# Kernel optimization log

Measured on AMD Instinct MI355X. Metric: run time of the kernel, lower is better.

## Reference

```python
import jax, jax.numpy as jnp
import numpy as np
import math

EMBED_DIM = 1024
N_HEADS = 16
QK_DIM = 64
V_DIM = 64
B, S = 4, 2048


def setup_inputs() -> dict:
    key = jax.random.key(0)
    ks = jax.random.split(key, 10)
    sc = lambda fan_in: 1.0 / math.sqrt(fan_in)
    X = jax.random.normal(ks[0], (B, S, EMBED_DIM), dtype=jnp.float32)
    mask = jax.random.randint(ks[1], (B, 1, S, S), 0, 2, dtype=jnp.int32)
    wQ = jax.random.uniform(ks[2], (EMBED_DIM, QK_DIM * N_HEADS), jnp.float32, -sc(EMBED_DIM), sc(EMBED_DIM))
    bQ = jnp.zeros((QK_DIM * N_HEADS,), jnp.float32)
    wK = jax.random.uniform(ks[3], (EMBED_DIM, QK_DIM * N_HEADS), jnp.float32, -sc(EMBED_DIM), sc(EMBED_DIM))
    bK = jnp.zeros((QK_DIM * N_HEADS,), jnp.float32)
    wV = jax.random.uniform(ks[4], (EMBED_DIM, V_DIM * N_HEADS), jnp.float32, -sc(EMBED_DIM), sc(EMBED_DIM))
    bV = jnp.zeros((V_DIM * N_HEADS,), jnp.float32)
    wO = jax.random.uniform(ks[5], (V_DIM * N_HEADS, EMBED_DIM), jnp.float32, -sc(V_DIM * N_HEADS), sc(V_DIM * N_HEADS))
    bO = jnp.zeros((EMBED_DIM,), jnp.float32)
    return {"X": X, "mask": mask, "wQ": wQ, "bQ": bQ, "wK": wK, "bK": bK,
            "wV": wV, "bV": bV, "wO": wO, "bO": bO}


def reference(X, mask, wQ, bQ, wK, bK, wV, bV, wO, bO):
    Bsz, Slen, _ = X.shape
    # projections -> [B, H, S, d]
    q = (X @ wQ + bQ).reshape(Bsz, Slen, N_HEADS, QK_DIM).transpose(0, 2, 1, 3)
    k = (X @ wK + bK).reshape(Bsz, Slen, N_HEADS, QK_DIM).transpose(0, 2, 1, 3)
    v = (X @ wV + bV).reshape(Bsz, Slen, N_HEADS, V_DIM).transpose(0, 2, 1, 3)
    # scores [B, H, S, S]
    scores = jnp.einsum("bhqd,bhkd->bhqk", q, k) / math.sqrt(QK_DIM)
    scores = jnp.where(mask == 0, jnp.float32(-1e9), scores)
    probs = jax.nn.softmax(scores, axis=-1)
    out = jnp.einsum("bhqk,bhkd->bhqd", probs, v)  # [B, H, S, v]
    out = out.transpose(0, 2, 1, 3).reshape(Bsz, Slen, N_HEADS * V_DIM)
    return out @ wO + bO
```

## Files before the change

### kernel.cpp

```cpp
#include <hip/hip_runtime.h>
#include <hip/hip_bf16.h>

#define EMB 1024
#define NH 16
#define DH 64
#define SEQ 2048

typedef __attribute__((ext_vector_type(8))) __bf16 bf16x8;
typedef __attribute__((ext_vector_type(4))) float f32x4;
typedef __attribute__((ext_vector_type(16))) float f32x16;

__device__ __forceinline__ void g2l16(const void* g, void* l) {
  __builtin_amdgcn_global_load_lds(
      (const __attribute__((address_space(1))) void*)g,
      (__attribute__((address_space(3))) void*)l, 16, 0, 0);
}

__global__ void detect_k(const unsigned short* __restrict__ xs,
                         int* __restrict__ flag) {
  __shared__ int cnt;
  if (threadIdx.x == 0) cnt = 0;
  __syncthreads();
  int hits = 0;
  for (int i = threadIdx.x; i < 16384; i += 256) {
    unsigned e = (xs[i] >> 7) & 0xFFu;
    if (e >= 0xC0u) hits++;
  }
  atomicAdd(&cnt, hits);
  __syncthreads();
  if (threadIdx.x == 0) *flag = (cnt > 16) ? 1 : 0;
}

__global__ void conv_k(const void* __restrict__ src,
                       __hip_bfloat16* __restrict__ dst,
                       const int* __restrict__ flag, int n4) {
  int i = blockIdx.x * 256 + threadIdx.x;
  if (i >= n4) return;
  if (*flag) {
    float4 v = ((const float4*)src)[i];
    ushort4 o;
    __hip_bfloat16 t;
    t = __float2bfloat16(v.x); o.x = *(unsigned short*)&t;
    t = __float2bfloat16(v.y); o.y = *(unsigned short*)&t;
    t = __float2bfloat16(v.z); o.z = *(unsigned short*)&t;
    t = __float2bfloat16(v.w); o.w = *(unsigned short*)&t;
    ((ushort4*)dst)[i] = o;
  } else {
    ((ushort4*)dst)[i] = ((const ushort4*)src)[i];
  }
}

__global__ void convB_k(const void* s0, const void* s1, const void* s2,
                        const void* s3, __hip_bfloat16* __restrict__ dst,
                        const int* __restrict__ flag) {
  const void* srcs[4] = {s0, s1, s2, s3};
  const void* src = srcs[blockIdx.x];
  int i = threadIdx.x;
  __hip_bfloat16* d = dst + blockIdx.x * 1024;
  if (*flag) {
    float4 v = ((const float4*)src)[i];
    ushort4 o;
    __hip_bfloat16 t;
    t = __float2bfloat16(v.x); o.x = *(unsigned short*)&t;
    t = __float2bfloat16(v.y); o.y = *(unsigned short*)&t;
    t = __float2bfloat16(v.z); o.z = *(unsigned short*)&t;
    t = __float2bfloat16(v.w); o.w = *(unsigned short*)&t;
    ((ushort4*)d)[i] = o;
  } else {
    ((ushort4*)d)[i] = ((const ushort4*)src)[i];
  }
}

__global__ void transW4_k(const void* s0, const void* s1, const void* s2,
                          const void* s3, __hip_bfloat16* d0,
                          __hip_bfloat16* d1, __hip_bfloat16* d2,
                          __hip_bfloat16* d3, const int* __restrict__ flag) {
  __shared__ __hip_bfloat16 tile[32][33];
  const void* srcs[4] = {s0, s1, s2, s3};
  __hip_bfloat16* dsts[4] = {d0, d1, d2, d3};
  const void* src = srcs[blockIdx.z];
  __hip_bfloat16* dst = dsts[blockIdx.z];
  int f = *flag;
  int tx = threadIdx.x, ty = threadIdx.y;
  int x = blockIdx.x * 32 + tx;
  int y0 = blockIdx.y * 32;
  for (int i = 0; i < 32; i += 8) {
    int idx = (y0 + ty + i) * EMB + x;
    tile[ty + i][tx] = f ? __float2bfloat16(((const float*)src)[idx])
                         : ((const __hip_bfloat16*)src)[idx];
  }
  __syncthreads();
  int x2 = y0 + tx;
  int y2 = blockIdx.x * 32;
  for (int i = 0; i < 32; i += 8)
    dst[(size_t)(y2 + ty + i) * EMB + x2] = tile[tx][ty + i];
}

__global__ void maskpack_k(const int* __restrict__ mask,
                           unsigned int* __restrict__ bits) {
  int g = blockIdx.x * 256 + threadIdx.x;
  int lane = threadIdx.x & 63;
  unsigned long long bal = __ballot(mask[g] != 0);
  if ((lane & 31) == 0)
    bits[g >> 5] = (unsigned int)(bal >> (lane & 32));
}

__launch_bounds__(256)
__global__ void gemm_qkv(const __hip_bfloat16* __restrict__ A,
                         const __hip_bfloat16* __restrict__ Bt,
                         const __hip_bfloat16* __restrict__ bias,
                         __hip_bfloat16* __restrict__ CQ,
                         __hip_bfloat16* __restrict__ CK,
                         __hip_bfloat16* __restrict__ CV) {
  __shared__ __align__(16) __bf16 sA[128 * 32];
  __shared__ __align__(16) __bf16 sB[128 * 32];
  const __bf16* Ab = (const __bf16*)A;
  const __bf16* Bb = (const __bf16*)Bt;

  int tid = threadIdx.x;
  int w = tid >> 6, lane = tid & 63;
  int quad = lane >> 4, lcol = lane & 15;
  int m0 = blockIdx.x * 128, n0 = blockIdx.y * 128;
  int wm = (w >> 1) * 64, wn = (w & 1) * 64;
  int region = n0 >> 10;

  f32x4 z = {0.f, 0.f, 0.f, 0.f};
  f32x4 acc[4][4];
#pragma unroll
  for (int i = 0; i < 4; i++)
#pragma unroll
    for (int j = 0; j < 4; j++) acc[i][j] = z;

  int c = w * 64 + lane;
  int r = c >> 2, cc = c & 3;

  for (int k0 = 0; k0 < 1024; k0 += 32) {
    __syncthreads();
    g2l16(Ab + (size_t)(m0 + r) * 1024 + k0 + cc * 8, (char*)sA + w * 1024);
    g2l16(Ab + (size_t)(m0 + r + 64) * 1024 + k0 + cc * 8, (char*)sA + 4096 + w * 1024);
    g2l16(Bb + (size_t)(n0 + r) * 1024 + k0 + cc * 8, (char*)sB + w * 1024);
    g2l16(Bb + (size_t)(n0 + r + 64) * 1024 + k0 + cc * 8, (char*)sB + 4096 + w * 1024);
    __syncthreads();

    bf16x8 af[4], bfr[4];
#pragma unroll
    for (int i = 0; i < 4; i++)
      af[i] = *(const bf16x8*)(sA + (wm + i * 16 + lcol) * 32 + quad * 8);
#pragma unroll
    for (int j = 0; j < 4; j++)
      bfr[j] = *(const bf16x8*)(sB + (wn + j * 16 + lcol) * 32 + quad * 8);
#pragma unroll
    for (int i = 0; i < 4; i++)
#pragma unroll
      for (int j = 0; j < 4; j++)
        acc[i][j] = __builtin_amdgcn_mfma_f32_16x16x32_bf16(af[i], bfr[j], acc[i][j], 0, 0, 0);
  }

  float scale = (region == 0) ? 0.18033688011111204f : 1.0f;
#pragma unroll
  for (int j = 0; j < 4; j++) {
    int col = n0 + wn + j * 16 + lcol;
    float bv = __bfloat162float(bias[col]);
    int lc = col & 1023;
    int h = lc >> 6, dd = lc & 63;
#pragma unroll
    for (int i = 0; i < 4; i++) {
      int rbase = m0 + wm + i * 16 + quad * 4;
      int b = rbase >> 11, s = rbase & 2047;
      if (region == 1) {
#pragma unroll
        for (int rr = 0; rr < 4; rr++) {
          float v = acc[i][j][rr] + bv;
          CK[(((size_t)(b * NH + h)) * SEQ + s + rr) * DH + dd] = __float2bfloat16(v);
        }
      } else {
        union { unsigned long long u; __hip_bfloat16 bb[4]; } pk;
#pragma unroll
        for (int rr = 0; rr < 4; rr++)
          pk.bb[rr] = __float2bfloat16((acc[i][j][rr] + bv) * scale);
        __hip_bfloat16* dst = (region == 0) ? CQ : CV;
        *(unsigned long long*)(dst + (((size_t)(b * NH + h)) * DH + dd) * SEQ + s) = pk.u;
      }
    }
  }
}

__launch_bounds__(256)
__global__ void gemm_o(const __hip_bfloat16* __restrict__ A,
                       const __hip_bfloat16* __restrict__ Bt,
                       const __hip_bfloat16* __restrict__ bias,
                       void* __restrict__ Cv, const int* __restrict__ flag) {
  __shared__ __align__(16) __bf16 sA[128 * 32];
  __shared__ __align__(16) __bf16 sB[128 * 32];
  const __bf16* Ab = (const __bf16*)A;
  const __bf16* Bb = (const __bf16*)Bt;
  int f32out = *flag;

  int tid = threadIdx.x;
  int w = tid >> 6, lane = tid & 63;
  int quad = lane >> 4, lcol = lane & 15;
  int m0 = blockIdx.x * 128, n0 = blockIdx.y * 128;
  int wm = (w >> 1) * 64, wn = (w & 1) * 64;

  f32x4 z = {0.f, 0.f, 0.f, 0.f};
  f32x4 acc[4][4];
#pragma unroll
  for (int i = 0; i < 4; i++)
#pragma unroll
    for (int j = 0; j < 4; j++) acc[i][j] = z;

  int c = w * 64 + lane;
  int r = c >> 2, cc = c & 3;

  for (int k0 = 0; k0 < 1024; k0 += 32) {
    __syncthreads();
    g2l16(Ab + (size_t)(m0 + r) * 1024 + k0 + cc * 8, (char*)sA + w * 1024);
    g2l16(Ab + (size_t)(m0 + r + 64) * 1024 + k0 + cc * 8, (char*)sA + 4096 + w * 1024);
    g2l16(Bb + (size_t)(n0 + r) * 1024 + k0 + cc * 8, (char*)sB + w * 1024);
    g2l16(Bb + (size_t)(n0 + r + 64) * 1024 + k0 + cc * 8, (char*)sB + 4096 + w * 1024);
    __syncthreads();

    bf16x8 af[4], bfr[4];
#pragma unroll
    for (int i = 0; i < 4; i++)
      af[i] = *(const bf16x8*)(sA + (wm + i * 16 + lcol) * 32 + quad * 8);
#pragma unroll
    for (int j = 0; j < 4; j++)
      bfr[j] = *(const bf16x8*)(sB + (wn + j * 16 + lcol) * 32 + quad * 8);
#pragma unroll
    for (int i = 0; i < 4; i++)
#pragma unroll
      for (int j = 0; j < 4; j++)
        acc[i][j] = __builtin_amdgcn_mfma_f32_16x16x32_bf16(af[i], bfr[j], acc[i][j], 0, 0, 0);
  }

#pragma unroll
  for (int j = 0; j < 4; j++) {
    int col = n0 + wn + j * 16 + lcol;
    float bv = __bfloat162float(bias[col]);
#pragma unroll
    for (int i = 0; i < 4; i++) {
      int rbase = m0 + wm + i * 16 + quad * 4;
#pragma unroll
      for (int rr = 0; rr < 4; rr++) {
        int m = rbase + rr;
        float v = acc[i][j][rr] + bv;
        if (f32out)
          ((float*)Cv)[(size_t)m * EMB + col] = v;
        else
          ((__hip_bfloat16*)Cv)[(size_t)m * EMB + col] = __float2bfloat16(v);
      }
    }
  }
}

__launch_bounds__(256, 4)
__global__ void attn_k(const __hip_bfloat16* __restrict__ Qt,
                       const __hip_bfloat16* __restrict__ Kp,
                       const __hip_bfloat16* __restrict__ Vp,
                       const unsigned int* __restrict__ mbits,
                       __hip_bfloat16* __restrict__ AO) {
  __shared__ __align__(16) __bf16 sK[2 * 64 * 64];
  __shared__ __align__(16) __bf16 sV[2 * 64 * 64];
  __shared__ unsigned long long sLut[16];

  int tid = threadIdx.x;
  int w = tid >> 6, lane = tid & 63, hi = lane >> 5, l31 = lane & 31;
  int swz7 = l31 & 7;
  int bid = blockIdx.x;
  int xcd = bid & 7, idx = bid >> 3;
  int bh = xcd * 8 + (idx >> 4);
  int qblk = idx & 15;
  int b = bh >> 4, h = bh & 15;

  if (tid < 16) {
    unsigned long long v = 0;
    if (tid & 1) v |= 0xFFFFull;
    if (tid & 2) v |= 0xFFFFull << 16;
    if (tid & 4) v |= 0xFFFFull << 32;
    if (tid & 8) v |= 0xFFFFull << 48;
    sLut[tid] = v;
  }

  const __bf16* Qb = (const __bf16*)Qt + (size_t)bh * DH * SEQ;
  const __bf16* Kb = (const __bf16*)Kp + (size_t)bh * SEQ * DH;
  const __bf16* Vb = (const __bf16*)Vp + (size_t)bh * DH * SEQ;
  int q_mine = qblk * 128 + w * 32 + l31;

  union { bf16x8 v; __bf16 e[8]; } qf[4];
#pragma unroll
  for (int s = 0; s < 4; s++)
#pragma unroll
    for (int j = 0; j < 8; j++)
      qf[s].e[j] = Qb[(size_t)(s * 16 + hi * 8 + j) * SEQ + q_mine];

  __bf16 onev = (__bf16)1.0f;
  bf16x8 ones = {onev, onev, onev, onev, onev, onev, onev, onev};

  f32x16 z16 = {0.f, 0.f, 0.f, 0.f, 0.f, 0.f, 0.f, 0.f,
                0.f, 0.f, 0.f, 0.f, 0.f, 0.f, 0.f, 0.f};
  f32x16 ot0 = z16, ot1 = z16;
  f32x16 lacc = z16;

  const unsigned long long* mrow =
      (const unsigned long long*)mbits + ((size_t)b * SEQ + q_mine) * (SEQ / 64);

  int kr = lane >> 3, pc = lane & 7;

  auto STAGE = [&](int buf, int kt) {
#pragma unroll
    for (int t2 = 0; t2 < 2; t2++) {
      int row = w * 16 + t2 * 8 + kr;
      g2l16(Kb + (size_t)(kt * 64 + row) * DH + (pc ^ kr) * 8,
            (char*)sK + buf * 8192 + (w * 16 + t2 * 8) * 128);
      g2l16(Vb + (size_t)row * SEQ + kt * 64 + (pc ^ kr) * 8,
            (char*)sV + buf * 8192 + (w * 16 + t2 * 8) * 128);
    }
  };

  STAGE(0, 0);
  unsigned long long mb = mrow[0];
  __syncthreads();

  for (int kt = 0; kt < SEQ / 64; ++kt) {
    int cur = kt & 1;
    const char* sKc = (const char*)sK + cur * 8192;
    const char* sVc = (const char*)sV + cur * 8192;
    if (kt < SEQ / 64 - 1) STAGE(cur ^ 1, kt + 1);
    unsigned long long mb_next = mrow[(kt + 1) & (SEQ / 64 - 1)];
    unsigned long long mbc = mb >> (4 * hi);

#pragma unroll
    for (int ct = 0; ct < 2; ct++) {
      f32x16 sc = z16;
      __builtin_amdgcn_s_setprio(1);
#pragma unroll
      for (int s = 0; s < 4; s++) {
        bf16x8 a = *(const bf16x8*)(sKc + ct * 4096 + l31 * 128 +
                                    (((2 * s + hi) ^ swz7) << 4));
        sc = __builtin_amdgcn_mfma_f32_32x32x16_bf16(a, qf[s].v, sc, 0, 0, 0);
      }
      __builtin_amdgcn_s_setprio(0);

      unsigned long long pr[4];
#pragma unroll
      for (int g = 0; g < 4; g++) {
        union { unsigned long long u; __bf16 bb[4]; } pk;
#pragma unroll
        for (int r = 0; r < 4; r++)
          pk.bb[r] = (__bf16)__builtin_amdgcn_exp2f(sc[4 * g + r]);
        unsigned nib = (unsigned)(mbc >> (32 * ct + 8 * g)) & 0xFu;
        pr[g] = pk.u & sLut[nib];
      }

      __builtin_amdgcn_s_setprio(1);
#pragma unroll
      for (int f2 = 0; f2 < 2; f2++) {
        int kb = 2 * ct + f2;
        union { bf16x8 v; unsigned long long d2[2]; } bp;
        bp.d2[0] = pr[2 * f2];
        bp.d2[1] = pr[2 * f2 + 1];
        int ch0 = ((2 * kb) ^ swz7) << 4;
        int ch1 = ((2 * kb + 1) ^ swz7) << 4;
        union { bf16x8 v; unsigned long long d2[2]; } av0, av1;
        const char* vr0 = sVc + l31 * 128 + 8 * hi;
        const char* vr1 = sVc + (32 + l31) * 128 + 8 * hi;
        av0.d2[0] = *(const unsigned long long*)(vr0 + ch0);
        av0.d2[1] = *(const unsigned long long*)(vr0 + ch1);
        av1.d2[0] = *(const unsigned long long*)(vr1 + ch0);
        av1.d2[1] = *(const unsigned long long*)(vr1 + ch1);
        ot0 = __builtin_amdgcn_mfma_f32_32x32x16_bf16(av0.v, bp.v, ot0, 0, 0, 0);
        ot1 = __builtin_amdgcn_mfma_f32_32x32x16_bf16(av1.v, bp.v, ot1, 0, 0, 0);
        lacc = __builtin_amdgcn_mfma_f32_32x32x16_bf16(ones, bp.v, lacc, 0, 0, 0);
      }
      __builtin_amdgcn_s_setprio(0);
    }

    mb = mb_next;
    __syncthreads();
  }

  float linv = 1.0f / fmaxf(lacc[0], 1e-20f);
#pragma unroll
  for (int dt = 0; dt < 2; dt++) {
    const f32x16& o = dt ? ot1 : ot0;
#pragma unroll
    for (int g = 0; g < 4; g++) {
      union { unsigned long long u; __hip_bfloat16 bb[4]; } pk;
#pragma unroll
      for (int r = 0; r < 4; r++)
        pk.bb[r] = __float2bfloat16(o[4 * g + r] * linv);
      *(unsigned long long*)((__bf16*)AO + ((size_t)b * SEQ + q_mine) * EMB +
                             h * 64 + dt * 32 + g * 8 + hi * 4) = pk.u;
    }
  }
}

extern "C" void kernel_launch(void* const* d_in, const int* in_sizes, int n_in,
                              void* d_out, int out_size, void* d_ws, size_t ws_size,
                              hipStream_t stream) {
  const int* mask = (const int*)d_in[1];

  char* ws = (char*)d_ws;
  int* flag             = (int*)ws;
  __hip_bfloat16* biasc = (__hip_bfloat16*)(ws + (64ull << 10));
  __hip_bfloat16* WQt   = (__hip_bfloat16*)(ws + (1ull << 20));
  __hip_bfloat16* WKt   = (__hip_bfloat16*)(ws + (3ull << 20));
  __hip_bfloat16* WVt   = (__hip_bfloat16*)(ws + (5ull << 20));
  __hip_bfloat16* WOt   = (__hip_bfloat16*)(ws + (7ull << 20));
  unsigned int* mbits   = (unsigned int*)(ws + (9ull << 20));
  __hip_bfloat16* Xc    = (__hip_bfloat16*)(ws + (12ull << 20));
  __hip_bfloat16* Qw    = (__hip_bfloat16*)(ws + (28ull << 20));
  __hip_bfloat16* Kw    = (__hip_bfloat16*)(ws + (44ull << 20));
  __hip_bfloat16* Vtw   = (__hip_bfloat16*)(ws + (60ull << 20));
  __hip_bfloat16* AO    = (__hip_bfloat16*)(ws + (76ull << 20));

  detect_k<<<1, 256, 0, stream>>>((const unsigned short*)d_in[0], flag);

  conv_k<<<8192, 256, 0, stream>>>(d_in[0], Xc, flag, 2097152);
  convB_k<<<4, 256, 0, stream>>>(d_in[3], d_in[5], d_in[7], d_in[9], biasc, flag);

  dim3 tb(32, 8);
  transW4_k<<<dim3(32, 32, 4), tb, 0, stream>>>(d_in[2], d_in[4], d_in[6],
                                                d_in[8], WQt, WKt, WVt, WOt, flag);
  maskpack_k<<<65536, 256, 0, stream>>>(mask, mbits);

  gemm_qkv<<<dim3(64, 24), 256, 0, stream>>>(Xc, WQt, biasc, Qw, Kw, Vtw);
  attn_k<<<dim3(1024), 256, 0, stream>>>(Qw, Kw, Vtw, mbits, AO);
  gemm_o<<<dim3(64, 8), 256, 0, stream>>>(AO, WOt, biasc + 3072, d_out, flag);
}
```

Before: 401.5 us.

## Load K fragments directly from global into registers instead of LDS

Removes the K tile staging through shared memory. Each lane now loads its K MFMA operands straight from global memory into registers, prefetching the next tile right after the current score MFMAs. This halves LDS usage and drops LDS reads for K, but every wave in the block redundantly fetches the same K data from global or L2. It also adds 8 bf16x8 registers per thread, which may pressure occupancy under launch_bounds(256,4).

```diff
diff --git a/kernel.cpp b/kernel.cpp
--- a/kernel.cpp
+++ b/kernel.cpp
@@ -260,7 +260,6 @@
                        const __hip_bfloat16* __restrict__ Vp,
                        const unsigned int* __restrict__ mbits,
                        __hip_bfloat16* __restrict__ AO) {
-  __shared__ __align__(16) __bf16 sK[2 * 64 * 64];
   __shared__ __align__(16) __bf16 sV[2 * 64 * 64];
   __shared__ unsigned long long sLut[16];
 
@@ -307,26 +306,35 @@
 
   int kr = lane >> 3, pc = lane & 7;
 
-  auto STAGE = [&](int buf, int kt) {
+  bf16x8 kf[8];
+  const __bf16* Krow = Kb + (size_t)l31 * DH + 8 * hi;
+  auto LOADK = [&](int kt2) {
+#pragma unroll
+    for (int ct = 0; ct < 2; ct++)
+#pragma unroll
+      for (int s = 0; s < 4; s++)
+        kf[ct * 4 + s] =
+            *(const bf16x8*)(Krow + (size_t)(kt2 * 64 + ct * 32) * DH + s * 16);
+  };
+
+  auto STAGEV = [&](int buf, int kt) {
 #pragma unroll
     for (int t2 = 0; t2 < 2; t2++) {
       int row = w * 16 + t2 * 8 + kr;
-      g2l16(Kb + (size_t)(kt * 64 + row) * DH + (pc ^ kr) * 8,
-            (char*)sK + buf * 8192 + (w * 16 + t2 * 8) * 128);
       g2l16(Vb + (size_t)row * SEQ + kt * 64 + (pc ^ kr) * 8,
             (char*)sV + buf * 8192 + (w * 16 + t2 * 8) * 128);
     }
   };
 
-  STAGE(0, 0);
+  LOADK(0);
+  STAGEV(0, 0);
   unsigned long long mb = mrow[0];
   __syncthreads();
 
   for (int kt = 0; kt < SEQ / 64; ++kt) {
     int cur = kt & 1;
-    const char* sKc = (const char*)sK + cur * 8192;
     const char* sVc = (const char*)sV + cur * 8192;
-    if (kt < SEQ / 64 - 1) STAGE(cur ^ 1, kt + 1);
+    if (kt < SEQ / 64 - 1) STAGEV(cur ^ 1, kt + 1);
     unsigned long long mb_next = mrow[(kt + 1) & (SEQ / 64 - 1)];
     unsigned long long mbc = mb >> (4 * hi);
 
@@ -335,12 +343,12 @@
       f32x16 sc = z16;
       __builtin_amdgcn_s_setprio(1);
 #pragma unroll
-      for (int s = 0; s < 4; s++) {
-        bf16x8 a = *(const bf16x8*)(sKc + ct * 4096 + l31 * 128 +
-                                    (((2 * s + hi) ^ swz7) << 4));
-        sc = __builtin_amdgcn_mfma_f32_32x32x16_bf16(a, qf[s].v, sc, 0, 0, 0);
-      }
+      for (int s = 0; s < 4; s++)
+        sc = __builtin_amdgcn_mfma_f32_32x32x16_bf16(kf[ct * 4 + s], qf[s].v,
+                                                     sc, 0, 0, 0);
       __builtin_amdgcn_s_setprio(0);
+
+      if (ct == 1 && kt < SEQ / 64 - 1) LOADK(kt + 1);
 
       unsigned long long pr[4];
 #pragma unroll
```

New measurement: 496.7 us. 23.7% more time.

## Fuse preprocessing kernels into one launch and swizzle GEMM block order

Applied to the files above, without the earlier changes.

The four preprocessing kernels (X conversion, bias conversion, weight transpose, mask bit-packing) become a single kernel that dispatches on block index ranges, removing three launches and the gaps between them. The QKV and output GEMMs switch to 1D grids with a swizzled block-to-tile mapping, so that workgroups launched close together touch different tiles, which is meant to change L2/cache locality across XCDs. The fused kernel declares shared memory for every block even though only the transpose blocks use it, and the swizzle alters scheduling in ways that may or may not help.

```diff
diff --git a/kernel.cpp b/kernel.cpp
--- a/kernel.cpp
+++ b/kernel.cpp
@@ -31,78 +31,80 @@
   if (threadIdx.x == 0) *flag = (cnt > 16) ? 1 : 0;
 }
 
-__global__ void conv_k(const void* __restrict__ src,
-                       __hip_bfloat16* __restrict__ dst,
-                       const int* __restrict__ flag, int n4) {
-  int i = blockIdx.x * 256 + threadIdx.x;
-  if (i >= n4) return;
-  if (*flag) {
-    float4 v = ((const float4*)src)[i];
-    ushort4 o;
-    __hip_bfloat16 t;
-    t = __float2bfloat16(v.x); o.x = *(unsigned short*)&t;
-    t = __float2bfloat16(v.y); o.y = *(unsigned short*)&t;
-    t = __float2bfloat16(v.z); o.z = *(unsigned short*)&t;
-    t = __float2bfloat16(v.w); o.w = *(unsigned short*)&t;
-    ((ushort4*)dst)[i] = o;
+__global__ void prep_k(const void* __restrict__ X, const int* __restrict__ mask,
+                       const void* wq, const void* bq, const void* wk,
+                       const void* bk, const void* wv, const void* bv,
+                       const void* wo, const void* bo,
+                       __hip_bfloat16* __restrict__ Xc,
+                       __hip_bfloat16* __restrict__ biasc,
+                       __hip_bfloat16* __restrict__ WQt,
+                       __hip_bfloat16* __restrict__ WKt,
+                       __hip_bfloat16* __restrict__ WVt,
+                       __hip_bfloat16* __restrict__ WOt,
+                       unsigned int* __restrict__ mbits,
+                       const int* __restrict__ flag) {
+  __shared__ __hip_bfloat16 tile[32][33];
+  int blk = blockIdx.x;
+  int tid = threadIdx.x;
+  int f = *flag;
+
+  if (blk < 8192) {
+    int i = blk * 256 + tid;
+    if (f) {
+      float4 v = ((const float4*)X)[i];
+      ushort4 o;
+      __hip_bfloat16 t;
+      t = __float2bfloat16(v.x); o.x = *(unsigned short*)&t;
+      t = __float2bfloat16(v.y); o.y = *(unsigned short*)&t;
+      t = __float2bfloat16(v.z); o.z = *(unsigned short*)&t;
+      t = __float2bfloat16(v.w); o.w = *(unsigned short*)&t;
+      ((ushort4*)Xc)[i] = o;
+    } else {
+      ((ushort4*)Xc)[i] = ((const ushort4*)X)[i];
+    }
+  } else if (blk < 8196) {
+    const void* srcs[4] = {bq, bk, bv, bo};
+    const void* src = srcs[blk - 8192];
+    __hip_bfloat16* d = biasc + (blk - 8192) * 1024;
+    if (f) {
+      float4 v = ((const float4*)src)[tid];
+      ushort4 o;
+      __hip_bfloat16 t;
+      t = __float2bfloat16(v.x); o.x = *(unsigned short*)&t;
+      t = __float2bfloat16(v.y); o.y = *(unsigned short*)&t;
+      t = __float2bfloat16(v.z); o.z = *(unsigned short*)&t;
+      t = __float2bfloat16(v.w); o.w = *(unsigned short*)&t;
+      ((ushort4*)d)[tid] = o;
+    } else {
+      ((ushort4*)d)[tid] = ((const ushort4*)src)[tid];
+    }
+  } else if (blk < 12292) {
+    int idx = blk - 8196;
+    int bx = idx & 31, byy = (idx >> 5) & 31, bz = idx >> 10;
+    const void* srcs[4] = {wq, wk, wv, wo};
+    __hip_bfloat16* dsts[4] = {WQt, WKt, WVt, WOt};
+    const void* src = srcs[bz];
+    __hip_bfloat16* dst = dsts[bz];
+    int tx = tid & 31, ty = tid >> 5;
+    int x = bx * 32 + tx;
+    int y0 = byy * 32;
+    for (int i = 0; i < 32; i += 8) {
+      int idx2 = (y0 + ty + i) * EMB + x;
+      tile[ty + i][tx] = f ? __float2bfloat16(((const float*)src)[idx2])
+                           : ((const __hip_bfloat16*)src)[idx2];
+    }
+    __syncthreads();
+    int x2 = y0 + tx;
+    int y2 = bx * 32;
+    for (int i = 0; i < 32; i += 8)
+      dst[(size_t)(y2 + ty + i) * EMB + x2] = tile[tx][ty + i];
   } else {
-    ((ushort4*)dst)[i] = ((const ushort4*)src)[i];
-  }
-}
-
-__global__ void convB_k(const void* s0, const void* s1, const void* s2,
-                        const void* s3, __hip_bfloat16* __restrict__ dst,
-                        const int* __restrict__ flag) {
-  const void* srcs[4] = {s0, s1, s2, s3};
-  const void* src = srcs[blockIdx.x];
-  int i = threadIdx.x;
-  __hip_bfloat16* d = dst + blockIdx.x * 1024;
-  if (*flag) {
-    float4 v = ((const float4*)src)[i];
-    ushort4 o;
-    __hip_bfloat16 t;
-    t = __float2bfloat16(v.x); o.x = *(unsigned short*)&t;
-    t = __float2bfloat16(v.y); o.y = *(unsigned short*)&t;
-    t = __float2bfloat16(v.z); o.z = *(unsigned short*)&t;
-    t = __float2bfloat16(v.w); o.w = *(unsigned short*)&t;
-    ((ushort4*)d)[i] = o;
-  } else {
-    ((ushort4*)d)[i] = ((const ushort4*)src)[i];
-  }
-}
-
-__global__ void transW4_k(const void* s0, const void* s1, const void* s2,
-                          const void* s3, __hip_bfloat16* d0,
-                          __hip_bfloat16* d1, __hip_bfloat16* d2,
-                          __hip_bfloat16* d3, const int* __restrict__ flag) {
-  __shared__ __hip_bfloat16 tile[32][33];
-  const void* srcs[4] = {s0, s1, s2, s3};
-  __hip_bfloat16* dsts[4] = {d0, d1, d2, d3};
-  const void* src = srcs[blockIdx.z];
-  __hip_bfloat16* dst = dsts[blockIdx.z];
-  int f = *flag;
-  int tx = threadIdx.x, ty = threadIdx.y;
-  int x = blockIdx.x * 32 + tx;
-  int y0 = blockIdx.y * 32;
-  for (int i = 0; i < 32; i += 8) {
-    int idx = (y0 + ty + i) * EMB + x;
-    tile[ty + i][tx] = f ? __float2bfloat16(((const float*)src)[idx])
-                         : ((const __hip_bfloat16*)src)[idx];
-  }
-  __syncthreads();
-  int x2 = y0 + tx;
-  int y2 = blockIdx.x * 32;
-  for (int i = 0; i < 32; i += 8)
-    dst[(size_t)(y2 + ty + i) * EMB + x2] = tile[tx][ty + i];
-}
-
-__global__ void maskpack_k(const int* __restrict__ mask,
-                           unsigned int* __restrict__ bits) {
-  int g = blockIdx.x * 256 + threadIdx.x;
-  int lane = threadIdx.x & 63;
-  unsigned long long bal = __ballot(mask[g] != 0);
-  if ((lane & 31) == 0)
-    bits[g >> 5] = (unsigned int)(bal >> (lane & 32));
+    int g = (blk - 12292) * 256 + tid;
+    int lane = tid & 63;
+    unsigned long long bal = __ballot(mask[g] != 0);
+    if ((lane & 31) == 0)
+      mbits[g >> 5] = (unsigned int)(bal >> (lane & 32));
+  }
 }
 
 __launch_bounds__(256)
@@ -120,7 +122,9 @@
   int tid = threadIdx.x;
   int w = tid >> 6, lane = tid & 63;
   int quad = lane >> 4, lcol = lane & 15;
-  int m0 = blockIdx.x * 128, n0 = blockIdx.y * 128;
+  int wg = blockIdx.x;
+  int swz = (wg & 7) * 192 + (wg >> 3);
+  int m0 = (swz & 63) * 128, n0 = (swz >> 6) * 128;
   int wm = (w >> 1) * 64, wn = (w & 1) * 64;
   int region = n0 >> 10;
 
@@ -199,7 +203,9 @@
   int tid = threadIdx.x;
   int w = tid >> 6, lane = tid & 63;
   int quad = lane >> 4, lcol = lane & 15;
-  int m0 = blockIdx.x * 128, n0 = blockIdx.y * 128;
+  int wg = blockIdx.x;
+  int swz = (wg & 7) * 64 + (wg >> 3);
+  int m0 = (swz & 63) * 128, n0 = (swz >> 6) * 128;
   int wm = (w >> 1) * 64, wn = (w & 1) * 64;
 
   f32x4 z = {0.f, 0.f, 0.f, 0.f};
@@ -417,15 +423,12 @@
 
   detect_k<<<1, 256, 0, stream>>>((const unsigned short*)d_in[0], flag);
 
-  conv_k<<<8192, 256, 0, stream>>>(d_in[0], Xc, flag, 2097152);
-  convB_k<<<4, 256, 0, stream>>>(d_in[3], d_in[5], d_in[7], d_in[9], biasc, flag);
-
-  dim3 tb(32, 8);
-  transW4_k<<<dim3(32, 32, 4), tb, 0, stream>>>(d_in[2], d_in[4], d_in[6],
-                                                d_in[8], WQt, WKt, WVt, WOt, flag);
-  maskpack_k<<<65536, 256, 0, stream>>>(mask, mbits);
-
-  gemm_qkv<<<dim3(64, 24), 256, 0, stream>>>(Xc, WQt, biasc, Qw, Kw, Vtw);
+  prep_k<<<77828, 256, 0, stream>>>(d_in[0], mask, d_in[2], d_in[3], d_in[4],
+                                    d_in[5], d_in[6], d_in[7], d_in[8],
+                                    d_in[9], Xc, biasc, WQt, WKt, WVt, WOt,
+                                    mbits, flag);
+
+  gemm_qkv<<<1536, 256, 0, stream>>>(Xc, WQt, biasc, Qw, Kw, Vtw);
   attn_k<<<dim3(1024), 256, 0, stream>>>(Qw, Kw, Vtw, mbits, AO);
-  gemm_o<<<dim3(64, 8), 256, 0, stream>>>(AO, WOt, biasc + 3072, d_out, flag);
-}
+  gemm_o<<<512, 256, 0, stream>>>(AO, WOt, biasc + 3072, d_out, flag);
+}
```

Result: no change. 408.3 us (+1.7%).
